# Performance work log

Hardware: AMD Instinct MI355X
Metric: run time of the kernel (lower is better)

Reference implementation:

```python
import jax, jax.numpy as jnp
import numpy as np

B, H, W, C = 4, 64, 64, 256
DQK = C // 8

def setup_inputs() -> dict:
    key = jax.random.key(0)
    kx, kq, kk, kv = jax.random.split(key, 4)
    x = jax.random.normal(kx, (B, H, W, C), dtype=jnp.float32)
    Wq = jax.random.normal(kq, (C, DQK), dtype=jnp.float32) * 0.05
    Wk = jax.random.normal(kk, (C, DQK), dtype=jnp.float32) * 0.05
    Wv = jax.random.normal(kv, (C, C), dtype=jnp.float32) * 0.05
    gamma = jnp.ones((1,), dtype=jnp.float32)  # nonzero so attention path matters
    return {"x": x, "Wq": Wq, "Wk": Wk, "Wv": Wv, "gamma": gamma}

def reference(x, Wq, Wk, Wv, gamma):
    b, h, w, c = x.shape
    n = h * w
    xf = x.reshape(b, n, c)                      # [B, N, C]
    q = jnp.einsum('bnc,cd->bnd', xf, Wq)        # [B, N, C/8]  (1x1 conv == GEMM)
    k = jnp.einsum('bnc,cd->bnd', xf, Wk)        # [B, N, C/8]
    v = jnp.einsum('bnc,ce->bne', xf, Wv)        # [B, N, C]
    scores = jnp.einsum('bnd,bmd->bnm', q, k)    # [B, N, N], no scaling (as in source)
    attn = jax.nn.softmax(scores, axis=-1)
    out = jnp.einsum('bnm,bme->bne', attn, v)    # [B, N, C]
    out = out.reshape(b, h, w, c)
    return x + gamma * out
```

## Files before the change

### kernel.cpp

```cpp
#include <hip/hip_runtime.h>
#include <stdint.h>

#define BB 4
#define NN 4096
#define CC 256
#define DD 32

typedef __bf16 bf16;
typedef bf16 bf16x4 __attribute__((ext_vector_type(4)));
typedef bf16 bf16x8 __attribute__((ext_vector_type(8)));
typedef float f32x4 __attribute__((ext_vector_type(4)));
typedef unsigned int u32x4 __attribute__((ext_vector_type(4)));

__global__ void prepw_kernel(const float* __restrict__ Wq,
                             const float* __restrict__ Wk,
                             const float* __restrict__ Wv,
                             bf16* __restrict__ WT)
{
    int i = blockIdx.x * 256 + threadIdx.x;
    if (i < 320 * 256) {
        int d = i >> 8, c = i & 255;
        float val;
        if (d < DD)          val = Wq[c * DD + d] * 1.4426950408889634f;
        else if (d < 2 * DD) val = Wk[c * DD + (d - DD)];
        else                 val = Wv[c * CC + (d - 2 * DD)];
        WT[i] = (bf16)val;
    }
}

__global__ __launch_bounds__(256) void proj_kernel(
    const float* __restrict__ x, const bf16* __restrict__ WT,
    bf16* __restrict__ qb, bf16* __restrict__ kb, bf16* __restrict__ vt)
{
    int b = blockIdx.x >> 7, nt = blockIdx.x & 127;
    int n0 = nt << 5;
    int tid = threadIdx.x;
    int w = tid >> 6, lane = tid & 63;
    int lm = lane & 15, g = lane >> 4;
    int rw = w >> 1;
    int ch = w & 1;

    f32x4 acc[10];
    f32x4 zero4 = {0.f, 0.f, 0.f, 0.f};
#pragma unroll
    for (int i = 0; i < 10; ++i) acc[i] = zero4;

    const float* xrow = x + ((size_t)(b * NN) + n0 + rw * 16 + lm) * CC;
    for (int kc = 0; kc < 8; ++kc) {
        f32x4 a0 = *(const f32x4*)(xrow + kc * 32 + g * 8);
        f32x4 a1 = *(const f32x4*)(xrow + kc * 32 + g * 8 + 4);
        bf16x8 a;
        a[0] = (bf16)a0[0]; a[1] = (bf16)a0[1]; a[2] = (bf16)a0[2]; a[3] = (bf16)a0[3];
        a[4] = (bf16)a1[0]; a[5] = (bf16)a1[1]; a[6] = (bf16)a1[2]; a[7] = (bf16)a1[3];
#pragma unroll
        for (int ct = 0; ct < 10; ++ct) {
            int ctg = ch * 10 + ct;
            bf16x8 wv = *(const bf16x8*)(WT + (ctg * 16 + lm) * 256 + kc * 32 + g * 8);
            acc[ct] = __builtin_amdgcn_mfma_f32_16x16x32_bf16(a, wv, acc[ct], 0, 0, 0);
        }
    }

#pragma unroll
    for (int ct = 0; ct < 10; ++ct) {
        int ctg = ch * 10 + ct;
        int col = ctg * 16 + lm;
        if (ctg < 4) {
#pragma unroll
            for (int r = 0; r < 4; ++r) {
                int n = n0 + rw * 16 + g * 4 + r;
                bf16 hv = (bf16)acc[ct][r];
                if (ctg < 2) qb[((size_t)(b * NN) + n) * DD + col] = hv;
                else         kb[((size_t)(b * NN) + n) * DD + (col - DD)] = hv;
            }
        } else {
            int c = col - 64;
            int tile = nt >> 1;
            int nbase = ((nt & 1) * 32 + rw * 16 + g * 4) ^ ((c & 7) << 3);
            bf16x4 pk;
            pk[0] = (bf16)acc[ct][0]; pk[1] = (bf16)acc[ct][1];
            pk[2] = (bf16)acc[ct][2]; pk[3] = (bf16)acc[ct][3];
            size_t off = (((size_t)(b * 64 + tile)) * 256 + c) * 64 + nbase;
            *(bf16x4*)(vt + off) = pk;
        }
    }
}


#define LOADK(KT_, KF) { \
    const bf16* kbase_ = kb + ((size_t)(b * NN) + (size_t)(KT_) * 64) * DD + g * 8; \
    KF[0] = *(const bf16x8*)(kbase_ + (lm +  0) * DD); \
    KF[1] = *(const bf16x8*)(kbase_ + (lm + 16) * DD); \
    KF[2] = *(const bf16x8*)(kbase_ + (lm + 32) * DD); \
    KF[3] = *(const bf16x8*)(kbase_ + (lm + 48) * DD); }

#define LOADV(KT_, VB) { \
    const bf16* vtile_ = vt + ((size_t)(b * 64 + (KT_))) * 16384; \
    _Pragma("unroll") \
    for (int ct_ = 0; ct_ < 4; ++ct_) { \
        int c_ = 64 * sub + 16 * ct_ + lm; \
        const bf16* vrow_ = vtile_ + c_ * 64; \
        int vsw_ = (c_ & 7) << 3; \
        VB[ct_][0] = *(const bf16x8*)(vrow_ + ((8 * g) ^ vsw_)); \
        VB[ct_][1] = *(const bf16x8*)(vrow_ + ((32 + 8 * g) ^ vsw_)); \
    } }

#define PVBLOCK(PRV_, VB) { \
    const float* alph_p = (const float*)(lds + 16384 + (PRV_) * 512); \
    const uint32_t* flg_p = (const uint32_t*)(lds + 16384 + (PRV_) * 512 + 256); \
    const unsigned char* Pp_ = lds + (PRV_) * 8192; \
    u32x4 fl_ = *(const u32x4*)flg_p; \
    if ((fl_[0] & fl_[1] & fl_[2] & fl_[3]) == 0u) { \
        _Pragma("unroll") for (int rt_ = 0; rt_ < 4; ++rt_) { \
            f32x4 a_ = *(const f32x4*)(alph_p + rt_ * 16 + 4 * g); \
            _Pragma("unroll") for (int ct_ = 0; ct_ < 4; ++ct_) { \
                acc[rt_][ct_][0] *= a_[0]; acc[rt_][ct_][1] *= a_[1]; \
                acc[rt_][ct_][2] *= a_[2]; acc[rt_][ct_][3] *= a_[3]; \
            } \
        } \
    } \
    int psw_ = (lm & 7) << 4; \
    __builtin_amdgcn_s_setprio(1); \
    _Pragma("unroll") for (int rt_ = 0; rt_ < 4; ++rt_) { \
        const unsigned char* pr_ = Pp_ + (rt_ * 16 + lm) * 128; \
        bf16x8 pa0_ = *(const bf16x8*)(pr_ + (( 0 + 16 * g) ^ psw_)); \
        bf16x8 pa1_ = *(const bf16x8*)(pr_ + ((64 + 16 * g) ^ psw_)); \
        _Pragma("unroll") for (int ct_ = 0; ct_ < 4; ++ct_) { \
            acc[rt_][ct_] = __builtin_amdgcn_mfma_f32_16x16x32_bf16(pa0_, VB[ct_][0], acc[rt_][ct_], 0, 0, 0); \
            acc[rt_][ct_] = __builtin_amdgcn_mfma_f32_16x16x32_bf16(pa1_, VB[ct_][1], acc[rt_][ct_], 0, 0, 0); \
        } \
    } \
    __builtin_amdgcn_s_setprio(0); \
}

#define PVSTEP(T_, VB) { \
    PVBLOCK((((T_) - 1) & 1), VB); \
    int ktn_ = ((T_) + 1 < 64) ? (T_) + 1 : 63; \
    LOADV(ktn_, VB); }

#define QKSTEP(T_, KF, KFN) { \
    const int cur_ = (T_) & 1; \
    f32x4 sv0 = __builtin_amdgcn_mfma_f32_16x16x32_bf16(KF[0], qf, zero4, 0, 0, 0); \
    f32x4 sv1 = __builtin_amdgcn_mfma_f32_16x16x32_bf16(KF[1], qf, zero4, 0, 0, 0); \
    f32x4 sv2 = __builtin_amdgcn_mfma_f32_16x16x32_bf16(KF[2], qf, zero4, 0, 0, 0); \
    f32x4 sv3 = __builtin_amdgcn_mfma_f32_16x16x32_bf16(KF[3], qf, zero4, 0, 0, 0); \
    int ktn_ = ((T_) + 1 < 64) ? (T_) + 1 : 63; \
    LOADK(ktn_, KFN); \
    float mx_ = fmaxf(fmaxf(fmaxf(sv0[0], sv0[1]), fmaxf(sv0[2], sv0[3])), \
                      fmaxf(fmaxf(sv1[0], sv1[1]), fmaxf(sv1[2], sv1[3]))); \
    mx_ = fmaxf(mx_, fmaxf(fmaxf(sv2[0], sv2[1]), fmaxf(sv2[2], sv2[3]))); \
    mx_ = fmaxf(mx_, fmaxf(fmaxf(sv3[0], sv3[1]), fmaxf(sv3[2], sv3[3]))); \
    mx_ = fmaxf(mx_, __shfl_xor(mx_, 16)); \
    mx_ = fmaxf(mx_, __shfl_xor(mx_, 32)); \
    float alpha_; \
    int wave_ok_ = __all(mx_ <= mrun + 11.5f); \
    if (!wave_ok_) { float mn_ = fmaxf(mrun, mx_); alpha_ = __builtin_exp2f(mrun - mn_); mrun = mn_; } \
    else alpha_ = 1.0f; \
    float ssum_; \
    { \
        _Pragma("unroll") for (int j_ = 0; j_ < 4; ++j_) sv0[j_] = __builtin_exp2f(sv0[j_] - mrun); \
        _Pragma("unroll") for (int j_ = 0; j_ < 4; ++j_) sv1[j_] = __builtin_exp2f(sv1[j_] - mrun); \
        _Pragma("unroll") for (int j_ = 0; j_ < 4; ++j_) sv2[j_] = __builtin_exp2f(sv2[j_] - mrun); \
        _Pragma("unroll") for (int j_ = 0; j_ < 4; ++j_) sv3[j_] = __builtin_exp2f(sv3[j_] - mrun); \
        f32x4 t_ = (sv0 + sv1) + (sv2 + sv3); \
        ssum_ = (t_[0] + t_[1]) + (t_[2] + t_[3]); \
        ssum_ += __shfl_xor(ssum_, 16); \
        ssum_ += __shfl_xor(ssum_, 32); \
    } \
    lrun = lrun * alpha_ + ssum_; \
    unsigned char* Pb_ = lds + cur_ * 8192; \
    { \
        int rb_ = (16 * sub + lm) * 128; \
        int sw_ = (lm & 7) << 4; \
        bf16x4 pk_; \
        pk_[0] = (bf16)sv0[0]; pk_[1] = (bf16)sv0[1]; pk_[2] = (bf16)sv0[2]; pk_[3] = (bf16)sv0[3]; \
        *(bf16x4*)(Pb_ + rb_ + (( 0 + 8 * g) ^ sw_)) = pk_; \
        pk_[0] = (bf16)sv1[0]; pk_[1] = (bf16)sv1[1]; pk_[2] = (bf16)sv1[2]; pk_[3] = (bf16)sv1[3]; \
        *(bf16x4*)(Pb_ + rb_ + ((32 + 8 * g) ^ sw_)) = pk_; \
        pk_[0] = (bf16)sv2[0]; pk_[1] = (bf16)sv2[1]; pk_[2] = (bf16)sv2[2]; pk_[3] = (bf16)sv2[3]; \
        *(bf16x4*)(Pb_ + rb_ + ((64 + 8 * g) ^ sw_)) = pk_; \
        pk_[0] = (bf16)sv3[0]; pk_[1] = (bf16)sv3[1]; pk_[2] = (bf16)sv3[2]; pk_[3] = (bf16)sv3[3]; \
        *(bf16x4*)(Pb_ + rb_ + ((96 + 8 * g) ^ sw_)) = pk_; \
    } \
    float* alph_ = (float*)(lds + 16384 + cur_ * 512); \
    uint32_t* flg_ = (uint32_t*)(lds + 16384 + cur_ * 512 + 256); \
    if (g == 0) alph_[16 * sub + lm] = alpha_; \
    if (lane == 0) flg_[sub] = (uint32_t)wave_ok_; \
    asm volatile("s_waitcnt lgkmcnt(0)" ::: "memory"); \
}

__global__ __launch_bounds__(512, 2) void attn_kernel(
    const bf16* __restrict__ qb, const bf16* __restrict__ kb,
    const bf16* __restrict__ vt, const float* __restrict__ x,
    const float* __restrict__ gamma, float* __restrict__ out)
{
    __shared__ __align__(16) unsigned char lds[17408];
    int bid = blockIdx.x;
    int xcd = bid & 7, slot = bid >> 3;
    int b = xcd >> 1;
    int qt = (xcd & 1) * 32 + slot;
    int n0 = qt << 6;
    int tid = threadIdx.x;
    int w = tid >> 6, lane = tid & 63;
    int lm = lane & 15, g = lane >> 4;
    int qk = (w & 1) == 0;
    int sub = w >> 1;

    f32x4 zero4 = {0.f, 0.f, 0.f, 0.f};
    f32x4 acc[4][4];
#pragma unroll
    for (int i = 0; i < 4; ++i)
#pragma unroll
        for (int j = 0; j < 4; ++j) acc[i][j] = zero4;
    float mrun = -1e30f, lrun = 0.f;

    bf16x8 qf{};
    bf16x8 kfA[4], kfB[4];
    bf16x8 vbA[4][2], vbB[4][2];

    if (qk) {
        qf = *(const bf16x8*)(qb + ((size_t)(b * NN) + n0 + sub * 16 + lm) * DD + g * 8);
        LOADK(0, kfA);
    } else {
        LOADV(0, vbA);
    }

    if (qk) { QKSTEP(0, kfA, kfB); }
    else    { LOADV(1, vbB); }
    __builtin_amdgcn_s_barrier();
    asm volatile("" ::: "memory");

    int kt = 1;
    while (kt <= 61) {
        if (qk) { QKSTEP(kt, kfB, kfA); } else { PVSTEP(kt, vbA); }
        __builtin_amdgcn_s_barrier();
        asm volatile("" ::: "memory");
        if (qk) { QKSTEP(kt + 1, kfA, kfB); } else { PVSTEP(kt + 1, vbB); }
        __builtin_amdgcn_s_barrier();
        asm volatile("" ::: "memory");
        kt += 2;
    }
    if (qk) { QKSTEP(63, kfB, kfA); } else { PVSTEP(63, vbA); }
    __builtin_amdgcn_s_barrier();
    asm volatile("" ::: "memory");

    float* lsh = (float*)(lds + 16384);
    if (qk && g == 0) lsh[16 * sub + lm] = lrun;
    asm volatile("s_waitcnt lgkmcnt(0)" ::: "memory");
    __builtin_amdgcn_s_barrier();
    asm volatile("" ::: "memory");

    if (!qk) {
        PVBLOCK(1, vbB);

        float gam = gamma[0];
#pragma unroll
        for (int rt = 0; rt < 4; ++rt) {
            f32x4 lv = *(const f32x4*)(lsh + rt * 16 + 4 * g);
            f32x4 inv;
            inv[0] = 1.f / lv[0]; inv[1] = 1.f / lv[1];
            inv[2] = 1.f / lv[2]; inv[3] = 1.f / lv[3];
#pragma unroll
            for (int ct = 0; ct < 4; ++ct) {
                int col = 64 * sub + 16 * ct + lm;
#pragma unroll
                for (int r = 0; r < 4; ++r) {
                    int n = n0 + rt * 16 + 4 * g + r;
                    size_t idx = ((size_t)(b * NN) + n) * CC + col;
                    out[idx] = x[idx] + gam * acc[rt][ct][r] * inv[r];
                }
            }
        }
    }
}

extern "C" void kernel_launch(void* const* d_in, const int* in_sizes, int n_in,
                              void* d_out, int out_size, void* d_ws, size_t ws_size,
                              hipStream_t stream)
{
    const float* x     = (const float*)d_in[0];
    const float* Wq    = (const float*)d_in[1];
    const float* Wk    = (const float*)d_in[2];
    const float* Wv    = (const float*)d_in[3];
    const float* gamma = (const float*)d_in[4];
    float* out = (float*)d_out;

    char* ws = (char*)d_ws;
    bf16* WT = (bf16*)(ws);
    bf16* qb = (bf16*)(ws + 163840);
    bf16* kb = (bf16*)(ws + 1212416);
    bf16* vt = (bf16*)(ws + 2260992);

    hipLaunchKernelGGL(prepw_kernel, dim3(320), dim3(256), 0, stream,
                       Wq, Wk, Wv, WT);
    hipLaunchKernelGGL(proj_kernel, dim3(512), dim3(256), 0, stream,
                       x, WT, qb, kb, vt);
    hipLaunchKernelGGL(attn_kernel, dim3(256), dim3(512), 0, stream,
                       qb, kb, vt, x, gamma, out);
}
```

Before: 98.51 us.

## Split key range across two wave groups and fuse QK and PV per wave

Replaces the producer/consumer split, where even waves computed QK softmax and odd waves did PV, with two groups of four waves. Each group processes half of the key tiles, and every wave does both the QK and PV MFMAs for its own rows. The two groups merge their partial results at the end through LDS using their running maxima and sums. The running max becomes wave-uniform, so per-step row-sum shuffles are dropped and the full max reduction only runs when a rescale is needed. This is meant to balance MFMA work and cut idle time between the specialised waves, at the cost of double the LDS and a bf16 exchange of partial accumulators, which loses some precision.

Result: slower. 102.9 us (+4.5%).

```diff
diff --git a/kernel.cpp b/kernel.cpp
--- a/kernel.cpp
+++ b/kernel.cpp
@@ -11,6 +11,10 @@
 typedef bf16 bf16x8 __attribute__((ext_vector_type(8)));
 typedef float f32x4 __attribute__((ext_vector_type(4)));
 typedef unsigned int u32x4 __attribute__((ext_vector_type(4)));
+
+__device__ __forceinline__ float fm3(float a, float b, float c) {
+    return fmaxf(fmaxf(a, b), c);
+}
 
 __global__ void prepw_kernel(const float* __restrict__ Wq,
                              const float* __restrict__ Wk,
@@ -97,7 +101,7 @@
     const bf16* vtile_ = vt + ((size_t)(b * 64 + (KT_))) * 16384; \
     _Pragma("unroll") \
     for (int ct_ = 0; ct_ < 4; ++ct_) { \
-        int c_ = 64 * sub + 16 * ct_ + lm; \
+        int c_ = 64 * wl + 16 * ct_ + lm; \
         const bf16* vrow_ = vtile_ + c_ * 64; \
         int vsw_ = (c_ & 7) << 3; \
         VB[ct_][0] = *(const bf16x8*)(vrow_ + ((8 * g) ^ vsw_)); \
@@ -105,9 +109,9 @@
     } }
 
 #define PVBLOCK(PRV_, VB) { \
-    const float* alph_p = (const float*)(lds + 16384 + (PRV_) * 512); \
-    const uint32_t* flg_p = (const uint32_t*)(lds + 16384 + (PRV_) * 512 + 256); \
-    const unsigned char* Pp_ = lds + (PRV_) * 8192; \
+    const float* alph_p = (const float*)(glds + 16384 + (PRV_) * 512); \
+    const uint32_t* flg_p = (const uint32_t*)(glds + 16384 + (PRV_) * 512 + 256); \
+    const unsigned char* Pp_ = glds + (PRV_) * 8192; \
     u32x4 fl_ = *(const u32x4*)flg_p; \
     if ((fl_[0] & fl_[1] & fl_[2] & fl_[3]) == 0u) { \
         _Pragma("unroll") for (int rt_ = 0; rt_ < 4; ++rt_) { \
@@ -119,7 +123,6 @@
         } \
     } \
     int psw_ = (lm & 7) << 4; \
-    __builtin_amdgcn_s_setprio(1); \
     _Pragma("unroll") for (int rt_ = 0; rt_ < 4; ++rt_) { \
         const unsigned char* pr_ = Pp_ + (rt_ * 16 + lm) * 128; \
         bf16x8 pa0_ = *(const bf16x8*)(pr_ + (( 0 + 16 * g) ^ psw_)); \
@@ -129,32 +132,40 @@
             acc[rt_][ct_] = __builtin_amdgcn_mfma_f32_16x16x32_bf16(pa1_, VB[ct_][1], acc[rt_][ct_], 0, 0, 0); \
         } \
     } \
-    __builtin_amdgcn_s_setprio(0); \
-}
-
-#define PVSTEP(T_, VB) { \
-    PVBLOCK((((T_) - 1) & 1), VB); \
-    int ktn_ = ((T_) + 1 < 64) ? (T_) + 1 : 63; \
-    LOADV(ktn_, VB); }
-
-#define QKSTEP(T_, KF, KFN) { \
+}
+
+#define STEP(T_, KF, KFN, VBP, DOPV) { \
     const int cur_ = (T_) & 1; \
+    __builtin_amdgcn_s_setprio(1); \
     f32x4 sv0 = __builtin_amdgcn_mfma_f32_16x16x32_bf16(KF[0], qf, zero4, 0, 0, 0); \
     f32x4 sv1 = __builtin_amdgcn_mfma_f32_16x16x32_bf16(KF[1], qf, zero4, 0, 0, 0); \
     f32x4 sv2 = __builtin_amdgcn_mfma_f32_16x16x32_bf16(KF[2], qf, zero4, 0, 0, 0); \
     f32x4 sv3 = __builtin_amdgcn_mfma_f32_16x16x32_bf16(KF[3], qf, zero4, 0, 0, 0); \
-    int ktn_ = ((T_) + 1 < 64) ? (T_) + 1 : 63; \
+    int ktn_ = ((T_) + 1) & 63;    \
     LOADK(ktn_, KFN); \
-    float mx_ = fmaxf(fmaxf(fmaxf(sv0[0], sv0[1]), fmaxf(sv0[2], sv0[3])), \
-                      fmaxf(fmaxf(sv1[0], sv1[1]), fmaxf(sv1[2], sv1[3]))); \
-    mx_ = fmaxf(mx_, fmaxf(fmaxf(sv2[0], sv2[1]), fmaxf(sv2[2], sv2[3]))); \
-    mx_ = fmaxf(mx_, fmaxf(fmaxf(sv3[0], sv3[1]), fmaxf(sv3[2], sv3[3]))); \
-    mx_ = fmaxf(mx_, __shfl_xor(mx_, 16)); \
-    mx_ = fmaxf(mx_, __shfl_xor(mx_, 32)); \
+    if (DOPV) { PVBLOCK(cur_ ^ 1, VBP); } \
+    __builtin_amdgcn_s_setprio(0); \
+    LOADV(ktn_, VBP); \
+    float mxa_ = fm3(sv0[0], sv0[1], sv0[2]); \
+    float mxb_ = fm3(sv0[3], sv1[0], sv1[1]); \
+    float mxc_ = fm3(sv1[2], sv1[3], sv2[0]); \
+    float mxd_ = fm3(sv2[1], sv2[2], sv2[3]); \
+    float mxe_ = fm3(sv3[0], sv3[1], sv3[2]); \
+    float mx_ = fmaxf(fm3(mxa_, mxb_, mxc_), fm3(mxd_, mxe_, sv3[3])); \
     float alpha_; \
     int wave_ok_ = __all(mx_ <= mrun + 11.5f); \
-    if (!wave_ok_) { float mn_ = fmaxf(mrun, mx_); alpha_ = __builtin_exp2f(mrun - mn_); mrun = mn_; } \
-    else alpha_ = 1.0f; \
+    if (!wave_ok_) { \
+        float wm_ = mx_; \
+        wm_ = fmaxf(wm_, __shfl_xor(wm_, 1)); \
+        wm_ = fmaxf(wm_, __shfl_xor(wm_, 2)); \
+        wm_ = fmaxf(wm_, __shfl_xor(wm_, 4)); \
+        wm_ = fmaxf(wm_, __shfl_xor(wm_, 8)); \
+        wm_ = fmaxf(wm_, __shfl_xor(wm_, 16)); \
+        wm_ = fmaxf(wm_, __shfl_xor(wm_, 32)); \
+        float mn_ = fmaxf(mrun, wm_); \
+        alpha_ = __builtin_exp2f(mrun - mn_); \
+        mrun = mn_; \
+    } else alpha_ = 1.0f; \
     float ssum_; \
     { \
         _Pragma("unroll") for (int j_ = 0; j_ < 4; ++j_) sv0[j_] = __builtin_exp2f(sv0[j_] - mrun); \
@@ -163,13 +174,11 @@
         _Pragma("unroll") for (int j_ = 0; j_ < 4; ++j_) sv3[j_] = __builtin_exp2f(sv3[j_] - mrun); \
         f32x4 t_ = (sv0 + sv1) + (sv2 + sv3); \
         ssum_ = (t_[0] + t_[1]) + (t_[2] + t_[3]); \
-        ssum_ += __shfl_xor(ssum_, 16); \
-        ssum_ += __shfl_xor(ssum_, 32); \
     } \
-    lrun = lrun * alpha_ + ssum_; \
-    unsigned char* Pb_ = lds + cur_ * 8192; \
+    lrun = lrun * alpha_ + ssum_;   \
+    unsigned char* Pb_ = glds + cur_ * 8192; \
     { \
-        int rb_ = (16 * sub + lm) * 128; \
+        int rb_ = (16 * wl + lm) * 128; \
         int sw_ = (lm & 7) << 4; \
         bf16x4 pk_; \
         pk_[0] = (bf16)sv0[0]; pk_[1] = (bf16)sv0[1]; pk_[2] = (bf16)sv0[2]; pk_[3] = (bf16)sv0[3]; \
@@ -181,11 +190,13 @@
         pk_[0] = (bf16)sv3[0]; pk_[1] = (bf16)sv3[1]; pk_[2] = (bf16)sv3[2]; pk_[3] = (bf16)sv3[3]; \
         *(bf16x4*)(Pb_ + rb_ + ((96 + 8 * g) ^ sw_)) = pk_; \
     } \
-    float* alph_ = (float*)(lds + 16384 + cur_ * 512); \
-    uint32_t* flg_ = (uint32_t*)(lds + 16384 + cur_ * 512 + 256); \
-    if (g == 0) alph_[16 * sub + lm] = alpha_; \
-    if (lane == 0) flg_[sub] = (uint32_t)wave_ok_; \
+    float* alph_ = (float*)(glds + 16384 + cur_ * 512); \
+    uint32_t* flg_ = (uint32_t*)(glds + 16384 + cur_ * 512 + 256); \
+    if (g == 0) alph_[16 * wl + lm] = alpha_; \
+    if (lane == 0) flg_[wl] = (uint32_t)wave_ok_; \
     asm volatile("s_waitcnt lgkmcnt(0)" ::: "memory"); \
+    __builtin_amdgcn_s_barrier(); \
+    asm volatile("" ::: "memory"); \
 }
 
 __global__ __launch_bounds__(512, 2) void attn_kernel(
@@ -193,7 +204,7 @@
     const bf16* __restrict__ vt, const float* __restrict__ x,
     const float* __restrict__ gamma, float* __restrict__ out)
 {
-    __shared__ __align__(16) unsigned char lds[17408];
+    __shared__ __align__(16) unsigned char lds[34816];
     int bid = blockIdx.x;
     int xcd = bid & 7, slot = bid >> 3;
     int b = xcd >> 1;
@@ -202,72 +213,97 @@
     int tid = threadIdx.x;
     int w = tid >> 6, lane = tid & 63;
     int lm = lane & 15, g = lane >> 4;
-    int qk = (w & 1) == 0;
-    int sub = w >> 1;
-
+    int grp = w >> 2;
+    int wl = w & 3;
+    unsigned char* glds = lds + grp * 17408;
+
+    bf16x8 qf = *(const bf16x8*)(qb + ((size_t)(b * NN) + n0 + wl * 16 + lm) * DD + g * 8);
+
+    f32x4 acc[4][4];
     f32x4 zero4 = {0.f, 0.f, 0.f, 0.f};
-    f32x4 acc[4][4];
 #pragma unroll
     for (int i = 0; i < 4; ++i)
 #pragma unroll
         for (int j = 0; j < 4; ++j) acc[i][j] = zero4;
     float mrun = -1e30f, lrun = 0.f;
 
-    bf16x8 qf{};
+    int kt0 = grp * 32;
+    int kt1 = kt0 + 32;
+
     bf16x8 kfA[4], kfB[4];
     bf16x8 vbA[4][2], vbB[4][2];
-
-    if (qk) {
-        qf = *(const bf16x8*)(qb + ((size_t)(b * NN) + n0 + sub * 16 + lm) * DD + g * 8);
-        LOADK(0, kfA);
-    } else {
-        LOADV(0, vbA);
-    }
-
-    if (qk) { QKSTEP(0, kfA, kfB); }
-    else    { LOADV(1, vbB); }
-    __builtin_amdgcn_s_barrier();
-    asm volatile("" ::: "memory");
-
-    int kt = 1;
-    while (kt <= 61) {
-        if (qk) { QKSTEP(kt, kfB, kfA); } else { PVSTEP(kt, vbA); }
-        __builtin_amdgcn_s_barrier();
-        asm volatile("" ::: "memory");
-        if (qk) { QKSTEP(kt + 1, kfA, kfB); } else { PVSTEP(kt + 1, vbB); }
-        __builtin_amdgcn_s_barrier();
-        asm volatile("" ::: "memory");
+    LOADK(kt0, kfA);
+    LOADV(kt0, vbA);
+
+    STEP(kt0, kfA, kfB, vbB, 0);
+
+    int kt = kt0 + 1;
+    while (kt + 2 <= kt1) {
+        STEP(kt,     kfB, kfA, vbA, 1);
+        STEP(kt + 1, kfA, kfB, vbB, 1);
         kt += 2;
     }
-    if (qk) { QKSTEP(63, kfB, kfA); } else { PVSTEP(63, vbA); }
-    __builtin_amdgcn_s_barrier();
-    asm volatile("" ::: "memory");
-
-    float* lsh = (float*)(lds + 16384);
-    if (qk && g == 0) lsh[16 * sub + lm] = lrun;
+    STEP(kt1 - 1, kfB, kfA, vbA, 1);
+    PVBLOCK(1, vbB);
+
+    lrun += __shfl_xor(lrun, 16);
+    lrun += __shfl_xor(lrun, 32);
+
     asm volatile("s_waitcnt lgkmcnt(0)" ::: "memory");
     __builtin_amdgcn_s_barrier();
     asm volatile("" ::: "memory");
 
-    if (!qk) {
-        PVBLOCK(1, vbB);
-
-        float gam = gamma[0];
-#pragma unroll
-        for (int rt = 0; rt < 4; ++rt) {
-            f32x4 lv = *(const f32x4*)(lsh + rt * 16 + 4 * g);
-            f32x4 inv;
-            inv[0] = 1.f / lv[0]; inv[1] = 1.f / lv[1];
-            inv[2] = 1.f / lv[2]; inv[3] = 1.f / lv[3];
+    float* lsh = (float*)(glds + 16384);
+    float* msh = (float*)(glds + 16384 + 256);
+    if (g == 0) lsh[16 * wl + lm] = lrun;
+    if (lane == 0) msh[wl] = mrun;
+    {
+        unsigned char* xout = glds + wl * 4096;
+        int rtbase = grp ? 0 : 2;
+#pragma unroll
+        for (int rr = 0; rr < 2; ++rr) {
 #pragma unroll
             for (int ct = 0; ct < 4; ++ct) {
-                int col = 64 * sub + 16 * ct + lm;
-#pragma unroll
-                for (int r = 0; r < 4; ++r) {
-                    int n = n0 + rt * 16 + 4 * g + r;
-                    size_t idx = ((size_t)(b * NN) + n) * CC + col;
-                    out[idx] = x[idx] + gam * acc[rt][ct][r] * inv[r];
-                }
+                f32x4 a4 = acc[rtbase + rr][ct];
+                bf16x4 p4;
+                p4[0] = (bf16)a4[0]; p4[1] = (bf16)a4[1];
+                p4[2] = (bf16)a4[2]; p4[3] = (bf16)a4[3];
+                *(bf16x4*)(xout + ((rr * 4 + ct) * 64 + g * 16 + lm) * 8) = p4;
+            }
+        }
+    }
+    asm volatile("s_waitcnt lgkmcnt(0)" ::: "memory");
+    __builtin_amdgcn_s_barrier();
+    asm volatile("" ::: "memory");
+
+    const unsigned char* oglds = lds + (grp ^ 1) * 17408;
+    const unsigned char* xin = oglds + wl * 4096;
+    const float* lo = (const float*)(oglds + 16384);
+    const float* mo = (const float*)(oglds + 16384 + 256);
+    float gam = gamma[0];
+    int rself = grp ? 2 : 0;
+#pragma unroll
+    for (int rr = 0; rr < 2; ++rr) {
+        int rt = rself + rr;
+        float mS = msh[rt], mO = mo[rt];
+        float M = fmaxf(mS, mO);
+        float wS = __builtin_exp2f(mS - M);
+        float wO = __builtin_exp2f(mO - M);
+        f32x4 lvS = *(const f32x4*)(lsh + rt * 16 + 4 * g);
+        f32x4 lvO = *(const f32x4*)(lo + rt * 16 + 4 * g);
+        f32x4 inv;
+#pragma unroll
+        for (int j = 0; j < 4; ++j) inv[j] = 1.f / (wS * lvS[j] + wO * lvO[j]);
+#pragma unroll
+        for (int ct = 0; ct < 4; ++ct) {
+            int col = 64 * wl + 16 * ct + lm;
+            bf16x4 ob = *(const bf16x4*)(xin + ((rr * 4 + ct) * 64 + g * 16 + lm) * 8);
+#pragma unroll
+            for (int r = 0; r < 4; ++r) {
+                int n = n0 + rt * 16 + 4 * g + r;
+                size_t idx = ((size_t)(b * NN) + n) * CC + col;
+                float merged = wS * acc[rt][ct][r] + wO * (float)ob[r];
+                out[idx] = x[idx] + gam * merged * inv[r];
             }
         }
     }
```
